# Kernel tuning notes

Hardware: AMD Instinct MI355X
Metric: run time of the kernel (lower is better)

The kernel has to match this reference:

```python
import jax, jax.numpy as jnp
import numpy as np

N_FFT = 100
CROP = int(np.ceil(N_FFT / 2))  # 50, non-redundant frequency components
D = 2 * CROP                    # MVN dimensionality
LOG_2PI = float(np.log(2.0 * np.pi))


def setup_inputs() -> dict:
    key = jax.random.key(0)
    B = 262144
    x = jax.random.normal(key, (B, N_FFT), dtype=jnp.float32)
    return {"x": x}


def reference(x):
    # Batched, vectorized equivalent of the per-sample numpy FFT loop:
    # fftshift(fft(x))[:CROP] / N_FFT, split into real/imag channels.
    X = jnp.fft.fftshift(jnp.fft.fft(x, axis=-1), axes=-1)[:, :CROP]  # [B, CROP] complex64
    x_fft = jnp.stack([jnp.real(X), jnp.imag(X)], axis=1) / N_FFT     # [B, 2, CROP] float32
    # Standard-normal MVN log-prob (zero mean, identity cov) over flattened [B, D].
    z = x_fft.reshape(x_fft.shape[0], -1)
    log_pz = -0.5 * jnp.sum(z * z, axis=-1) - 0.5 * D * LOG_2PI       # [B]
    # log_jacob is the constant 0 in the original module; omitted as non-tensor.
    return (x_fft, log_pz)
```

## Files before the change

### kernel.cpp

```cpp
#include <hip/hip_runtime.h>
#include <hip/hip_bf16.h>
#include <math.h>


#define NFFT  100
#define CROP  50
#define BLOCK 256
#define TM    64
#define WN    112
#define WK    128
#define CSTR  108
#define LOGPZ_CONST -91.893853320467274f

typedef short  bf16x8 __attribute__((ext_vector_type(8)));
typedef float  f32x4  __attribute__((ext_vector_type(4)));

__device__ unsigned short g_Wbf[WN * WK];

static __device__ inline short f2b(float f) {
    __hip_bfloat16 h = __float2bfloat16(f);
    return *reinterpret_cast<short*>(&h);
}

__global__ void init_w_kernel() {
    int idx = blockIdx.x * blockDim.x + threadIdx.x;
    if (idx < WN * WK) {
        int j = idx / WK;
        int k = idx - j * WK;
        float v = 0.0f;
        if (j < NFFT && k < NFFT) {
            int bin = (j < CROP) ? (CROP + j) : j;
            int t = (bin * k) % NFFT;
            float ang = (float)t * 0.06283185307179586477f;
            v = ((j < CROP) ? cosf(ang) : -sinf(ang)) * 0.01f;
        }
        g_Wbf[idx] = (unsigned short)f2b(v);
    }
}

__global__ __launch_bounds__(BLOCK) void dft_kernel(const float* __restrict__ x,
                                                    float* __restrict__ out,
                                                    int B) {
    __shared__ float cst[TM * CSTR];
    __shared__ float p2[TM];

    const int tid  = threadIdx.x;
    const int lane = tid & 63;
    const int wv   = tid >> 6;
    const int lr   = lane & 15;
    const int kb   = lane >> 4;

    const int rbase = blockIdx.x * TM + wv * 16 + lr;
    const float* __restrict__ xr = x + (size_t)rbase * NFFT;

    bf16x8 afr[4];
#pragma unroll
    for (int kg = 0; kg < 3; ++kg) {
        const float4* p = reinterpret_cast<const float4*>(xr + kg * 32 + kb * 8);
        float4 u0 = p[0];
        float4 u1 = p[1];
        bf16x8 a;
        a[0] = f2b(u0.x); a[1] = f2b(u0.y); a[2] = f2b(u0.z); a[3] = f2b(u0.w);
        a[4] = f2b(u1.x); a[5] = f2b(u1.y); a[6] = f2b(u1.z); a[7] = f2b(u1.w);
        afr[kg] = a;
    }
    {
        float4 u = make_float4(0.f, 0.f, 0.f, 0.f);
        if (kb == 0) u = *reinterpret_cast<const float4*>(xr + 96);
        bf16x8 a;
        a[0] = f2b(u.x); a[1] = f2b(u.y); a[2] = f2b(u.z); a[3] = f2b(u.w);
        a[4] = 0; a[5] = 0; a[6] = 0; a[7] = 0;
        afr[3] = a;
    }

    const unsigned short* __restrict__ W = g_Wbf;
    f32x4 acc[7];
#pragma unroll
    for (int nt = 0; nt < 7; ++nt) acc[nt] = (f32x4){0.f, 0.f, 0.f, 0.f};

#pragma unroll
    for (int nt = 0; nt < 7; ++nt) {
        const unsigned short* wrow = W + (size_t)(nt * 16 + lr) * WK + kb * 8;
#pragma unroll
        for (int kg = 0; kg < 4; ++kg) {
            bf16x8 bfr = *reinterpret_cast<const bf16x8*>(wrow + kg * 32);
            acc[nt] = __builtin_amdgcn_mfma_f32_16x16x32_bf16(afr[kg], bfr, acc[nt], 0, 0, 0);
        }
    }

    float s2[4] = {0.f, 0.f, 0.f, 0.f};
#pragma unroll
    for (int nt = 0; nt < 7; ++nt) {
        int col = nt * 16 + lr;
        if (col < NFFT) {
#pragma unroll
            for (int i = 0; i < 4; ++i) {
                float v = acc[nt][i];
                cst[(wv * 16 + kb * 4 + i) * CSTR + col] = v;
                s2[i] = fmaf(v, v, s2[i]);
            }
        }
    }

#pragma unroll
    for (int i = 0; i < 4; ++i) {
        float t = s2[i];
        t += __shfl_xor(t, 1, 64);
        t += __shfl_xor(t, 2, 64);
        t += __shfl_xor(t, 4, 64);
        t += __shfl_xor(t, 8, 64);
        if (lr == 0) p2[wv * 16 + kb * 4 + i] = t;
    }

    __syncthreads();

    float* __restrict__ dst = out + (size_t)blockIdx.x * TM * NFFT;
#pragma unroll
    for (int i = 0; i < 25; ++i) {
        int e  = tid + i * BLOCK;
        int rr = e / NFFT;
        int cc = e - rr * NFFT;
        dst[e] = cst[rr * CSTR + cc];
    }
    if (tid < TM) {
        out[(size_t)B * NFFT + blockIdx.x * TM + tid] =
            fmaf(p2[tid], -0.5f, LOGPZ_CONST);
    }
}

extern "C" void kernel_launch(void* const* d_in, const int* in_sizes, int n_in,
                              void* d_out, int out_size, void* d_ws, size_t ws_size,
                              hipStream_t stream) {
    const float* x = (const float*)d_in[0];
    float* out = (float*)d_out;
    const int B = in_sizes[0] / NFFT;

    hipLaunchKernelGGL(init_w_kernel, dim3((WN * WK + BLOCK - 1) / BLOCK),
                       dim3(BLOCK), 0, stream);
    hipLaunchKernelGGL(dft_kernel, dim3(B / TM), dim3(BLOCK), 0, stream, x, out, B);
}
```

Measured before the change: 216.5 us.

## Process several row tiles per block with register prefetch and per-wave stores

Each block now loops over four 64-row tiles instead of one. While the current tile's MFMAs run, the next tile's input is loaded into registers, so global load latency overlaps with compute. The block-wide barrier and the shared log-prob buffer are gone: each wave copies its own 16 rows out of LDS and writes log_pz straight from the shuffle reduction. The grid is four times smaller, which lowers the number of resident waves available to hide memory latency and adds register pressure from the prefetch buffers.

```diff
diff --git a/kernel.cpp b/kernel.cpp
--- a/kernel.cpp
+++ b/kernel.cpp
@@ -7,6 +7,7 @@
 #define CROP  50
 #define BLOCK 256
 #define TM    64
+#define T     4
 #define WN    112
 #define WK    128
 #define CSTR  108
@@ -42,7 +43,6 @@
                                                     float* __restrict__ out,
                                                     int B) {
     __shared__ float cst[TM * CSTR];
-    __shared__ float p2[TM];
 
     const int tid  = threadIdx.x;
     const int lane = tid & 63;
@@ -50,81 +50,104 @@
     const int lr   = lane & 15;
     const int kb   = lane >> 4;
 
-    const int rbase = blockIdx.x * TM + wv * 16 + lr;
-    const float* __restrict__ xr = x + (size_t)rbase * NFFT;
+    const int rowInBlk = wv * 16 + lr;
+    const size_t blkBase = (size_t)blockIdx.x * (TM * T);
+    const unsigned short* __restrict__ W = g_Wbf;
 
+    float4 ld[7];
     bf16x8 afr[4];
+
+    {
+        const float* __restrict__ xr = x + (blkBase + rowInBlk) * NFFT;
 #pragma unroll
-    for (int kg = 0; kg < 3; ++kg) {
-        const float4* p = reinterpret_cast<const float4*>(xr + kg * 32 + kb * 8);
-        float4 u0 = p[0];
-        float4 u1 = p[1];
-        bf16x8 a;
-        a[0] = f2b(u0.x); a[1] = f2b(u0.y); a[2] = f2b(u0.z); a[3] = f2b(u0.w);
-        a[4] = f2b(u1.x); a[5] = f2b(u1.y); a[6] = f2b(u1.z); a[7] = f2b(u1.w);
-        afr[kg] = a;
-    }
-    {
-        float4 u = make_float4(0.f, 0.f, 0.f, 0.f);
-        if (kb == 0) u = *reinterpret_cast<const float4*>(xr + 96);
-        bf16x8 a;
-        a[0] = f2b(u.x); a[1] = f2b(u.y); a[2] = f2b(u.z); a[3] = f2b(u.w);
-        a[4] = 0; a[5] = 0; a[6] = 0; a[7] = 0;
-        afr[3] = a;
+        for (int kg = 0; kg < 3; ++kg) {
+            const float4* p = reinterpret_cast<const float4*>(xr + kg * 32 + kb * 8);
+            ld[2 * kg]     = p[0];
+            ld[2 * kg + 1] = p[1];
+        }
+        ld[6] = *reinterpret_cast<const float4*>(xr + 96);
     }
 
-    const unsigned short* __restrict__ W = g_Wbf;
-    f32x4 acc[7];
+    for (int t = 0; t < T; ++t) {
 #pragma unroll
-    for (int nt = 0; nt < 7; ++nt) acc[nt] = (f32x4){0.f, 0.f, 0.f, 0.f};
+        for (int kg = 0; kg < 3; ++kg) {
+            float4 u0 = ld[2 * kg], u1 = ld[2 * kg + 1];
+            bf16x8 a;
+            a[0] = f2b(u0.x); a[1] = f2b(u0.y); a[2] = f2b(u0.z); a[3] = f2b(u0.w);
+            a[4] = f2b(u1.x); a[5] = f2b(u1.y); a[6] = f2b(u1.z); a[7] = f2b(u1.w);
+            afr[kg] = a;
+        }
+        {
+            float4 u = ld[6];
+            bf16x8 a;
+            a[0] = f2b(u.x); a[1] = f2b(u.y); a[2] = f2b(u.z); a[3] = f2b(u.w);
+            a[4] = 0; a[5] = 0; a[6] = 0; a[7] = 0;
+            afr[3] = a;
+        }
+
+        if (t + 1 < T) {
+            const float* __restrict__ xr =
+                x + (blkBase + (size_t)(t + 1) * TM + rowInBlk) * NFFT;
+#pragma unroll
+            for (int kg = 0; kg < 3; ++kg) {
+                const float4* p = reinterpret_cast<const float4*>(xr + kg * 32 + kb * 8);
+                ld[2 * kg]     = p[0];
+                ld[2 * kg + 1] = p[1];
+            }
+            ld[6] = *reinterpret_cast<const float4*>(xr + 96);
+        }
+
+        f32x4 acc[7];
+#pragma unroll
+        for (int nt = 0; nt < 7; ++nt) acc[nt] = (f32x4){0.f, 0.f, 0.f, 0.f};
+#pragma unroll
+        for (int nt = 0; nt < 7; ++nt) {
+            const unsigned short* wrow = W + (size_t)(nt * 16 + lr) * WK + kb * 8;
+#pragma unroll
+            for (int kg = 0; kg < 4; ++kg) {
+                bf16x8 bfr = *reinterpret_cast<const bf16x8*>(wrow + kg * 32);
+                acc[nt] = __builtin_amdgcn_mfma_f32_16x16x32_bf16(afr[kg], bfr, acc[nt], 0, 0, 0);
+            }
+        }
+
+        float s2[4] = {0.f, 0.f, 0.f, 0.f};
+#pragma unroll
+        for (int nt = 0; nt < 7; ++nt) {
+            int col = nt * 16 + lr;
+            if (col < NFFT) {
+#pragma unroll
+                for (int i = 0; i < 4; ++i) {
+                    float v = acc[nt][i];
+                    cst[(wv * 16 + kb * 4 + i) * CSTR + col] = v;
+                    s2[i] = fmaf(v, v, s2[i]);
+                }
+            }
+        }
+
+        const size_t tileBase = blkBase + (size_t)t * TM;
 
 #pragma unroll
-    for (int nt = 0; nt < 7; ++nt) {
-        const unsigned short* wrow = W + (size_t)(nt * 16 + lr) * WK + kb * 8;
-#pragma unroll
-        for (int kg = 0; kg < 4; ++kg) {
-            bf16x8 bfr = *reinterpret_cast<const bf16x8*>(wrow + kg * 32);
-            acc[nt] = __builtin_amdgcn_mfma_f32_16x16x32_bf16(afr[kg], bfr, acc[nt], 0, 0, 0);
-        }
-    }
-
-    float s2[4] = {0.f, 0.f, 0.f, 0.f};
-#pragma unroll
-    for (int nt = 0; nt < 7; ++nt) {
-        int col = nt * 16 + lr;
-        if (col < NFFT) {
-#pragma unroll
-            for (int i = 0; i < 4; ++i) {
-                float v = acc[nt][i];
-                cst[(wv * 16 + kb * 4 + i) * CSTR + col] = v;
-                s2[i] = fmaf(v, v, s2[i]);
+        for (int i = 0; i < 4; ++i) {
+            float r = s2[i];
+            r += __shfl_xor(r, 1, 64);
+            r += __shfl_xor(r, 2, 64);
+            r += __shfl_xor(r, 4, 64);
+            r += __shfl_xor(r, 8, 64);
+            if (lr == 0) {
+                out[(size_t)B * NFFT + tileBase + wv * 16 + kb * 4 + i] =
+                    fmaf(r, -0.5f, LOGPZ_CONST);
             }
         }
-    }
 
+        const float* __restrict__ csrc = cst + wv * 16 * CSTR;
+        float* __restrict__ dstw = out + (tileBase + wv * 16) * NFFT;
 #pragma unroll
-    for (int i = 0; i < 4; ++i) {
-        float t = s2[i];
-        t += __shfl_xor(t, 1, 64);
-        t += __shfl_xor(t, 2, 64);
-        t += __shfl_xor(t, 4, 64);
-        t += __shfl_xor(t, 8, 64);
-        if (lr == 0) p2[wv * 16 + kb * 4 + i] = t;
-    }
-
-    __syncthreads();
-
-    float* __restrict__ dst = out + (size_t)blockIdx.x * TM * NFFT;
-#pragma unroll
-    for (int i = 0; i < 25; ++i) {
-        int e  = tid + i * BLOCK;
-        int rr = e / NFFT;
-        int cc = e - rr * NFFT;
-        dst[e] = cst[rr * CSTR + cc];
-    }
-    if (tid < TM) {
-        out[(size_t)B * NFFT + blockIdx.x * TM + tid] =
-            fmaf(p2[tid], -0.5f, LOGPZ_CONST);
+        for (int i = 0; i < 25; ++i) {
+            int e  = lane + i * 64;
+            int rr = e / NFFT;
+            int cc = e - rr * NFFT;
+            dstw[e] = csrc[rr * CSTR + cc];
+        }
     }
 }
 
@@ -137,5 +160,6 @@
 
     hipLaunchKernelGGL(init_w_kernel, dim3((WN * WK + BLOCK - 1) / BLOCK),
                        dim3(BLOCK), 0, stream);
-    hipLaunchKernelGGL(dft_kernel, dim3(B / TM), dim3(BLOCK), 0, stream, x, out, B);
+    hipLaunchKernelGGL(dft_kernel, dim3(B / (TM * T)), dim3(BLOCK), 0, stream,
+                       x, out, B);
 }
```

Result: faster. 200.5 us (-7.4%).
